# Kernel optimization log

Measured on AMD Instinct MI355X. Metric: run time of the kernel, lower is better.

## Reference

```python
import jax, jax.numpy as jnp
import numpy as np

D_MODEL = 256
D_INNER = 512   # expand=2 * d_model
D_STATE = 16
D_CONV = 4
DT_RANK = 16    # ceil(d_model/16)
N_BLOCKS = 5
BATCH = 8192
INPUT_DIM = 2048
NUM_CLASSES = 8


def setup_inputs() -> dict:
    key = jax.random.key(0)
    ks = jax.random.split(key, 10)
    rn = lambda k, shape, s: jax.random.normal(k, shape, jnp.float32) * s
    inp = {}
    inp['x'] = rn(ks[0], (BATCH, INPUT_DIM), 1.0)
    # preprocess Linear(input_dim, 256)
    inp['W_pre'] = rn(ks[1], (D_MODEL, INPUT_DIM), 0.02)
    inp['b_pre'] = jnp.zeros((D_MODEL,), jnp.float32)
    # per-block Mamba params, stacked over N_BLOCKS
    inp['in_proj_w'] = rn(ks[2], (N_BLOCKS, 2 * D_INNER, D_MODEL), 0.02)
    inp['conv_w'] = rn(ks[3], (N_BLOCKS, D_INNER, 1, D_CONV), 0.1)   # depthwise, groups=d_inner
    inp['conv_b'] = jnp.zeros((N_BLOCKS, D_INNER), jnp.float32)
    inp['x_proj_w'] = rn(ks[4], (N_BLOCKS, DT_RANK + 2 * D_STATE, D_INNER), 0.02)
    inp['dt_proj_w'] = rn(ks[5], (N_BLOCKS, D_INNER, DT_RANK), 0.1)
    inp['dt_proj_b'] = rn(ks[6], (N_BLOCKS, D_INNER), 0.1)
    # S4D-real init: A = 1..d_state, A_log = log(A)
    A = jnp.tile(jnp.arange(1, D_STATE + 1, dtype=jnp.float32)[None, None, :], (N_BLOCKS, D_INNER, 1))
    inp['A_log'] = jnp.log(A)
    inp['D'] = jnp.ones((N_BLOCKS, D_INNER), jnp.float32)
    inp['out_proj_w'] = rn(ks[7], (N_BLOCKS, D_MODEL, D_INNER), 0.02)
    inp['ln_g'] = jnp.ones((D_MODEL,), jnp.float32)
    inp['ln_b'] = jnp.zeros((D_MODEL,), jnp.float32)
    inp['W_cls'] = rn(ks[8], (NUM_CLASSES, D_MODEL), 0.02)
    inp['b_cls'] = jnp.zeros((NUM_CLASSES,), jnp.float32)
    return inp


def _mamba(x, in_w, cw, cb, xw, dtw, dtb, Alog, Dp, ow):
    # x: (B, L, d_model)
    B, L, _ = x.shape
    xz = jnp.einsum('bld,ed->ble', x, in_w)            # (B, L, 2*d_inner)
    xi, z = jnp.split(xz, 2, axis=-1)
    # causal depthwise conv1d over the sequence axis
    xt = xi.transpose(0, 2, 1)                         # (B, d_inner, L)
    xc = jax.lax.conv_general_dilated(
        xt, cw, window_strides=(1,), padding=[(D_CONV - 1, 0)],
        dimension_numbers=('NCH', 'OIH', 'NCH'), feature_group_count=D_INNER)
    xi = jax.nn.silu((xc + cb[None, :, None]).transpose(0, 2, 1))   # (B, L, d_inner)
    xdbl = jnp.einsum('bld,ed->ble', xi, xw)           # (B, L, dt_rank + 2*d_state)
    dt, Bm, Cm = jnp.split(xdbl, [DT_RANK, DT_RANK + D_STATE], axis=-1)
    dt = jax.nn.softplus(jnp.einsum('blr,dr->bld', dt, dtw) + dtb)  # (B, L, d_inner)
    A = -jnp.exp(Alog)                                  # (d_inner, d_state)
    dA = jnp.exp(dt[..., None] * A)                     # (B, L, d_inner, d_state)
    dBx = dt[..., None] * Bm[:, :, None, :] * xi[..., None]

    def step(h, t):
        dA_t, dBx_t, C_t = t
        h = dA_t * h + dBx_t                            # (B, d_inner, d_state)
        return h, jnp.einsum('bds,bs->bd', h, C_t)

    h0 = jnp.zeros((B, D_INNER, D_STATE), x.dtype)
    _, ys = jax.lax.scan(step, h0, (dA.swapaxes(0, 1), dBx.swapaxes(0, 1), Cm.swapaxes(0, 1)))
    y = ys.swapaxes(0, 1) + xi * Dp                     # (B, L, d_inner)
    y = y * jax.nn.silu(z)
    return jnp.einsum('bld,ed->ble', y, ow)             # (B, L, d_model)


def reference(x, W_pre, b_pre, in_proj_w, conv_w, conv_b, x_proj_w, dt_proj_w,
              dt_proj_b, A_log, D, out_proj_w, ln_g, ln_b, W_cls, b_cls):
    # dropout is identity in eval mode
    h = (x @ W_pre.T + b_pre)[:, None, :]               # (B, 1, 256)
    for i in range(N_BLOCKS):
        h = h + _mamba(h, in_proj_w[i], conv_w[i], conv_b[i], x_proj_w[i],
                       dt_proj_w[i], dt_proj_b[i], A_log[i], D[i], out_proj_w[i])
    mu = h.mean(-1, keepdims=True)
    var = ((h - mu) ** 2).mean(-1, keepdims=True)
    hn = (h - mu) * jax.lax.rsqrt(var + 1e-5) * ln_g + ln_b
    return hn[:, 0, :] @ W_cls.T + b_cls                # (B, num_classes)
```

## Files before the change

### kernel.cpp

```cpp
#include <hip/hip_runtime.h>
#include <hip/hip_bf16.h>

typedef __attribute__((ext_vector_type(8))) short bf16x8;
typedef __attribute__((ext_vector_type(4))) short s16x4;
typedef __attribute__((ext_vector_type(4))) float f32x4;
typedef __attribute__((ext_vector_type(4))) float float4v;

static __device__ __forceinline__ unsigned short f2b(float f) {
  unsigned int u = __builtin_bit_cast(unsigned int, f);
  u += 0x7fffu + ((u >> 16) & 1u);
  return (unsigned short)(u >> 16);
}
static __device__ __forceinline__ float b2f(unsigned short s) {
  unsigned int u = ((unsigned int)s) << 16;
  return __builtin_bit_cast(float, u);
}
static __device__ __forceinline__ float fsilu(float x) {
  float e = __builtin_amdgcn_exp2f(-1.44269504f * x);
  return x * __builtin_amdgcn_rcpf(1.f + e);
}
static __device__ __forceinline__ float fsoftplus(float a) {
  if (a > 20.f) return a;
  float t = __builtin_amdgcn_exp2f(1.44269504f * a);
  return 0.69314718f * __builtin_amdgcn_logf(1.f + t);
}
static __device__ __forceinline__ void gl16(const void* g, void* l) {
  __builtin_amdgcn_global_load_lds(
      (const __attribute__((address_space(1))) unsigned int*)g,
      (__attribute__((address_space(3))) unsigned int*)l, 16, 0, 0);
}
template <int N>
static __device__ __forceinline__ void waitv() {
  if constexpr (N == 0) asm volatile("s_waitcnt vmcnt(0)" ::: "memory");
  else if constexpr (N == 1) asm volatile("s_waitcnt vmcnt(1)" ::: "memory");
  else if constexpr (N == 2) asm volatile("s_waitcnt vmcnt(2)" ::: "memory");
  else if constexpr (N == 3) asm volatile("s_waitcnt vmcnt(3)" ::: "memory");
  else if constexpr (N == 4) asm volatile("s_waitcnt vmcnt(4)" ::: "memory");
  else if constexpr (N == 5) asm volatile("s_waitcnt vmcnt(5)" ::: "memory");
  else if constexpr (N == 6) asm volatile("s_waitcnt vmcnt(6)" ::: "memory");
  else if constexpr (N == 8) asm volatile("s_waitcnt vmcnt(8)" ::: "memory");
}
static __device__ __forceinline__ void lgkm_bar() {
  asm volatile("s_waitcnt lgkmcnt(0)" ::: "memory");
  __builtin_amdgcn_s_barrier();
}

template <int TM, int TN>
__global__ __launch_bounds__(256) void gemm_pl(
    const unsigned short* __restrict__ A, const unsigned short* __restrict__ W,
    int N, int K, int GY,
    const float* __restrict__ p0, float* __restrict__ of,
    unsigned short* __restrict__ ob) {
  constexpr int FM = TM / 32, FN = TN / 32;
  constexpr int IA = TM / 64, IW = TN / 64;
  constexpr int LPT = IA + IW;
  __shared__ __align__(16) unsigned short As[4][TM * 32];
  __shared__ __align__(16) unsigned short Ws[4][TN * 32];

  const int t = threadIdx.x, lane = t & 63, wave = t >> 6;
  const int lr = lane & 15;
  const int q = gridDim.x >> 3;
  const int s = (blockIdx.x & 7) * q + (blockIdx.x >> 3);
  const int bm = (s / GY) * TM, bn = (s % GY) * TN;
  const int wr = (wave >> 1) * (TM / 2), wc = (wave & 1) * (TN / 2);

  f32x4 acc[FM][FN];
#pragma unroll
  for (int i = 0; i < FM; ++i)
#pragma unroll
    for (int j = 0; j < FN; ++j) acc[i][j] = (f32x4){0.f, 0.f, 0.f, 0.f};

  const unsigned short* agB =
      A + (long)(bm + wave * (TM / 4) + (lane >> 2)) * K +
      ((lane & 3) ^ ((lane >> 3) & 3)) * 8;
  const unsigned short* wgB =
      W + (long)(bn + wave * (TN / 4) + (lane >> 2)) * K +
      ((lane & 3) ^ ((lane >> 3) & 3)) * 8;

  auto STAGE = [&](int k0, int b) {
#pragma unroll
    for (int j = 0; j < IA; ++j)
      gl16(agB + k0 + (long)j * 16 * K, &As[b][(wave * (TM / 4) + j * 16) * 32]);
#pragma unroll
    for (int j = 0; j < IW; ++j)
      gl16(wgB + k0 + (long)j * 16 * K, &Ws[b][(wave * (TN / 4) + j * 16) * 32]);
  };

  auto COMPUTE = [&](int b) {
    bf16x8 af[FM], bg[FN];
    const int sw = ((lane >> 4) ^ ((lane >> 1) & 3)) * 8;
#pragma unroll
    for (int m = 0; m < FM; ++m)
      af[m] = *(const bf16x8*)&As[b][(wr + m * 16 + lr) * 32 + sw];
#pragma unroll
    for (int n = 0; n < FN; ++n)
      bg[n] = *(const bf16x8*)&Ws[b][(wc + n * 16 + lr) * 32 + sw];
    __builtin_amdgcn_s_setprio(1);
#pragma unroll
    for (int m = 0; m < FM; ++m)
#pragma unroll
      for (int n = 0; n < FN; ++n)
        acc[m][n] = __builtin_amdgcn_mfma_f32_16x16x32_bf16(af[m], bg[n],
                                                            acc[m][n], 0, 0, 0);
    __builtin_amdgcn_s_setprio(0);
  };

  const int NT = K >> 5;
  STAGE(0, 0);
  STAGE(32, 1);
  for (int tt = 0; tt < NT; ++tt) {
    if (tt + 2 < NT) {
      STAGE((tt + 2) << 5, (tt + 2) & 3);
      waitv<2 * LPT>();
    } else if (tt + 1 < NT) {
      waitv<LPT>();
    } else {
      waitv<0>();
    }
    __builtin_amdgcn_s_barrier();
    COMPUTE(tt & 3);
    __builtin_amdgcn_sched_barrier(0);
  }

  const int m0 = bm + wr + (lane >> 4) * 4;
  const int n0 = bn + wc + lr;
#pragma unroll
  for (int mi = 0; mi < FM; ++mi)
#pragma unroll
    for (int ni = 0; ni < FN; ++ni) {
      const int n = n0 + ni * 16;
#pragma unroll
      for (int r = 0; r < 4; ++r) {
        const int m = m0 + mi * 16 + r;
        float v = acc[mi][ni][r] + p0[n];
        of[(long)m * N + n] = v;
        ob[(long)m * N + n] = f2b(v);
      }
    }
}

__global__ __launch_bounds__(512) void mamba5(
    const unsigned short* __restrict__ hb0, const float* __restrict__ h0,
    const unsigned short* __restrict__ inwb,
    const unsigned short* __restrict__ xwpb,
    const unsigned short* __restrict__ dtwpb,
    const unsigned short* __restrict__ owb,
    const float* __restrict__ conv_b, const float* __restrict__ dt_b,
    const float* __restrict__ Dp,
    const float* __restrict__ ln_g, const float* __restrict__ ln_b,
    const float* __restrict__ Wc, const float* __restrict__ bc,
    float* __restrict__ out) {
  __shared__ __align__(16) unsigned short SMEM[81216];
  unsigned short* XiL = SMEM;
  unsigned short* SzL = SMEM + 16384;
  unsigned short* Ring = SMEM + 32768;
  unsigned short* HLr = SMEM + 65536;
  float* Dxl = (float*)(SMEM + 73728);
  float* BCl = (float*)(SMEM + 78080);
  float* Par = (float*)(SMEM + 78144);

  const int t = threadIdx.x, lane = t & 63, w = t >> 6;
  const int lr = lane & 15, lg = lane >> 4;
  const int bm = blockIdx.x * 32;
  const int m04 = lg * 4;
  const int rg16 = (w >> 2) * 16;
  const int cg32 = (w & 3) * 32;
  const int strow = lane >> 2;
  const int stc = (lane & 3) ^ ((strow >> 1) & 3);

#pragma unroll
  for (int j = 0; j < 2; ++j) {
    const int i = w * 2 + j;
    const int row = 2 * i + (lane >> 5);
    const int c = (lane & 31) ^ (row & 7);
    gl16(hb0 + (long)(bm + row) * 256 + c * 8, HLr + i * 512);
  }
  float hres[2][2][4];
#pragma unroll
  for (int ng = 0; ng < 2; ++ng)
#pragma unroll
    for (int n = 0; n < 2; ++n)
#pragma unroll
      for (int r = 0; r < 4; ++r)
        hres[ng][n][r] = h0[(long)(bm + rg16 + m04 + r) * 256 + ng * 128 +
                            cg32 + n * 16 + lr];
  waitv<0>();
  __builtin_amdgcn_s_barrier();

  for (int blk = 0; blk < 5; ++blk) {
    const unsigned short* inw = inwb + (long)blk * 1024 * 256;
    const unsigned short* xwp = xwpb + (long)blk * 64 * 512;
    const unsigned short* dtwp = dtwpb + (long)blk * 512 * 32;
    const unsigned short* ow = owb + (long)blk * 256 * 512;
    const float* cbv = conv_b + blk * 512;
    const float* dtbv = dt_b + blk * 512;
    const float* Dv = Dp + blk * 512;

    auto STAGE1 = [&](int tt, int slot) {
      const int nt = tt >> 3, kq = tt & 7;
      gl16(inw + (long)(nt * 128 + w * 16 + strow) * 256 + kq * 32 + stc * 8,
           Ring + slot * 4096 + w * 512);
    };
    if (w < 6) {
      const float* ps = (w < 2) ? cbv + (w & 1) * 256
                      : (w < 4) ? dtbv + (w & 1) * 256
                                : Dv + (w & 1) * 256;
      gl16(ps + lane * 4, (unsigned short*)Par + w * 512);
    }
    STAGE1(0, 0); STAGE1(1, 1); STAGE1(2, 2); STAGE1(3, 3);
    STAGE1(4, 4); STAGE1(5, 5); STAGE1(6, 6);
    f32x4 acc1[2];
#pragma unroll
    for (int tt = 0; tt < 64; ++tt) {
      if (tt <= 57) waitv<6>();
      else if (tt == 58) waitv<5>();
      else if (tt == 59) waitv<4>();
      else if (tt == 60) waitv<3>();
      else if (tt == 61) waitv<2>();
      else if (tt == 62) waitv<1>();
      else waitv<0>();
      __builtin_amdgcn_s_barrier();
      if (tt + 7 < 64) STAGE1(tt + 7, (tt + 7) & 7);
      __builtin_amdgcn_sched_barrier(0);
      const int nt = tt >> 3, kq = tt & 7;
      if (kq == 0) {
#pragma unroll
        for (int n = 0; n < 2; ++n) {
          const int c = nt * 128 + cg32 + n * 16 + lr;
          const float cb = (nt < 4) ? Par[c] : 0.f;
          acc1[n] = (f32x4){cb, cb, cb, cb};
        }
      }
      const unsigned short* Bs = Ring + (tt & 7) * 4096;
      const int ar = rg16 + lr;
      bf16x8 af = *(const bf16x8*)
          &HLr[ar * 256 + (((kq * 4 + lg) ^ (ar & 7)) * 8)];
      bf16x8 bg[2];
#pragma unroll
      for (int n = 0; n < 2; ++n) {
        const int rb = cg32 + n * 16 + lr;
        bg[n] = *(const bf16x8*)&Bs[rb * 32 + ((lg ^ ((rb >> 1) & 3)) * 8)];
      }
      __builtin_amdgcn_s_setprio(1);
#pragma unroll
      for (int n = 0; n < 2; ++n)
        acc1[n] = __builtin_amdgcn_mfma_f32_16x16x32_bf16(af, bg[n], acc1[n],
                                                          0, 0, 0);
      __builtin_amdgcn_s_setprio(0);
      if (kq == 7) {
#pragma unroll
        for (int n = 0; n < 2; ++n) {
          const int c = nt * 128 + cg32 + n * 16 + lr;
#pragma unroll
          for (int r = 0; r < 4; ++r) {
            const int row = rg16 + m04 + r;
            const float v = fsilu(acc1[n][r]);
            if (nt < 4) {
              XiL[row * 512 + (((c >> 3) ^ (row & 7)) * 8) + (c & 7)] = f2b(v);
            } else {
              const int cs = c - 512;
              SzL[row * 512 + (((cs >> 3) ^ (row & 7)) * 8) + (cs & 7)] =
                  f2b(v);
            }
          }
        }
      }
      __builtin_amdgcn_sched_barrier(0);
    }
#pragma unroll
    for (int j = 0; j < 6; ++j) {
      const int i = w * 6 + j;
      gl16(xwp + (long)i * 512 + (lane ^ (i & 7)) * 8, Ring + i * 512);
    }
    lgkm_bar();

#pragma unroll
    for (int j = 0; j < 2; ++j) {
      const int u = w * 2 + j;
      const int row = u * 16 + (lane >> 2);
      const int c = (lane & 3) ^ (row & 3);
      gl16(dtwp + (long)row * 32 + c * 8, Ring + 24576 + u * 512);
    }
    waitv<2>();
    __builtin_amdgcn_s_barrier();
    {
      const int fm2 = w & 1, fn2 = w >> 1;
      const int ar = fm2 * 16 + lr, rb = fn2 * 16 + lr;
      f32x4 a2 = {0.f, 0.f, 0.f, 0.f};
      __builtin_amdgcn_s_setprio(1);
#pragma unroll
      for (int kc = 0; kc < 16; ++kc) {
        bf16x8 af = *(const bf16x8*)
            &XiL[ar * 512 + (((kc * 4 + lg) ^ (lr & 7)) * 8)];
        bf16x8 bg = *(const bf16x8*)
            &Ring[rb * 512 + (((kc * 4 + lg) ^ (lr & 7)) * 8)];
        a2 = __builtin_amdgcn_mfma_f32_16x16x32_bf16(af, bg, a2, 0, 0, 0);
      }
      __builtin_amdgcn_s_setprio(0);
#pragma unroll
      for (int r = 0; r < 4; ++r)
        Dxl[(fm2 * 16 + m04 + r) * 68 + fn2 * 16 + lr] = a2[r];
    }
    lgkm_bar();

#pragma unroll
    for (int j = 0; j < 2; ++j) {
      const int u = w * 2 + j;
      const int row = 256 + u * 16 + (lane >> 2);
      const int c = (lane & 3) ^ (row & 3);
      gl16(dtwp + (long)row * 32 + c * 8, Ring + u * 512);
    }
    if (t < 32) {
      float bc2 = 0.f;
      const float* dx = &Dxl[t * 68];
#pragma unroll
      for (int s2 = 0; s2 < 16; ++s2) bc2 += dx[16 + s2] * dx[32 + s2];
      BCl[t] = bc2;
    }
    bf16x8 afdt;
    {
      const float* dx = &Dxl[((w & 1) * 16 + lr) * 68 + lg * 8];
#pragma unroll
      for (int e = 0; e < 8; ++e) afdt[e] = (short)f2b(dx[e]);
    }
    waitv<0>();
    lgkm_bar();

    {
      const int fn4 = w >> 1, m04b = (w & 1) * 16 + m04;
#pragma unroll
      for (int tt = 0; tt < 8; ++tt) {
        const int d = tt * 64 + fn4 * 16 + lr;
        const unsigned short* dbase = (tt < 4) ? (Ring + 24576) : Ring;
        const int doff = (tt < 4) ? d : (d - 256);
        bf16x8 bg =
            *(const bf16x8*)&dbase[doff * 32 + ((lg ^ (d & 3)) * 8)];
        f32x4 da = __builtin_amdgcn_mfma_f32_16x16x32_bf16(
            afdt, bg, (f32x4){0.f, 0.f, 0.f, 0.f}, 0, 0, 0);
        const float dbv = Par[512 + d], dvv = Par[1024 + d];
#pragma unroll
        for (int r = 0; r < 4; ++r) {
          const int row = m04b + r;
          const float dtv = fsoftplus(da[r] + dbv);
          const int xoff = row * 512 + (((d >> 3) ^ (row & 7)) * 8) + (d & 7);
          const float y = b2f(XiL[xoff]) * (dtv * BCl[row] + dvv) *
                          b2f(SzL[xoff]);
          XiL[xoff] = f2b(y);
        }
      }
    }
    lgkm_bar();

    auto STAGE5 = [&](int tt, int slot) {
      const int ng = tt >> 4, kq = tt & 15;
      gl16(ow + (long)(ng * 128 + w * 16 + strow) * 512 + kq * 32 + stc * 8,
           Ring + slot * 4096 + w * 512);
    };
    STAGE5(0, 0); STAGE5(1, 1); STAGE5(2, 2); STAGE5(3, 3);
    STAGE5(4, 4); STAGE5(5, 5); STAGE5(6, 6);
    f32x4 acc5[2];
#pragma unroll
    for (int tt = 0; tt < 32; ++tt) {
      if (tt <= 25) waitv<6>();
      else if (tt == 26) waitv<5>();
      else if (tt == 27) waitv<4>();
      else if (tt == 28) waitv<3>();
      else if (tt == 29) waitv<2>();
      else if (tt == 30) waitv<1>();
      else waitv<0>();
      __builtin_amdgcn_s_barrier();
      if (tt + 7 < 32) STAGE5(tt + 7, (tt + 7) & 7);
      __builtin_amdgcn_sched_barrier(0);
      const int ng = tt >> 4, kq = tt & 15;
      if (kq == 0) {
        acc5[0] = (f32x4){0.f, 0.f, 0.f, 0.f};
        acc5[1] = (f32x4){0.f, 0.f, 0.f, 0.f};
      }
      const unsigned short* Bs = Ring + (tt & 7) * 4096;
      const int ar = rg16 + lr;
      bf16x8 af = *(const bf16x8*)
          &XiL[ar * 512 + (((kq * 4 + lg) ^ (ar & 7)) * 8)];
      bf16x8 bg[2];
#pragma unroll
      for (int n = 0; n < 2; ++n) {
        const int rb = cg32 + n * 16 + lr;
        bg[n] = *(const bf16x8*)&Bs[rb * 32 + ((lg ^ ((rb >> 1) & 3)) * 8)];
      }
      __builtin_amdgcn_s_setprio(1);
#pragma unroll
      for (int n = 0; n < 2; ++n)
        acc5[n] = __builtin_amdgcn_mfma_f32_16x16x32_bf16(af, bg[n], acc5[n],
                                                          0, 0, 0);
      __builtin_amdgcn_s_setprio(0);
      if (kq == 15) {
#pragma unroll
        for (int n = 0; n < 2; ++n) {
          const int col = ng * 128 + cg32 + n * 16 + lr;
#pragma unroll
          for (int r = 0; r < 4; ++r) {
            const int row = rg16 + m04 + r;
            const float v = acc5[n][r] + hres[ng][n][r];
            hres[ng][n][r] = v;
            HLr[row * 256 + (((col >> 3) ^ (row & 7)) * 8) + (col & 7)] =
                f2b(v);
          }
        }
      }
      __builtin_amdgcn_sched_barrier(0);
    }
    lgkm_bar();
  }

  {
    float* Rf = (float*)Ring;
#pragma unroll
    for (int ng = 0; ng < 2; ++ng)
#pragma unroll
      for (int n = 0; n < 2; ++n)
#pragma unroll
        for (int r = 0; r < 4; ++r)
          Rf[(rg16 + m04 + r) * 256 + ng * 128 + cg32 + n * 16 + lr] =
              hres[ng][n][r];
    lgkm_bar();
#pragma unroll
    for (int rr = 0; rr < 4; ++rr) {
      const int row = w * 4 + rr;
      float4v v = ((const float4v*)(Rf + row * 256))[lane];
      float s = v[0] + v[1] + v[2] + v[3];
#pragma unroll
      for (int o = 32; o; o >>= 1) s += __shfl_xor(s, o);
      const float mu = s * (1.f / 256.f);
      float d0 = v[0] - mu, d1 = v[1] - mu, d2 = v[2] - mu, d3 = v[3] - mu;
      float qq = d0 * d0 + d1 * d1 + d2 * d2 + d3 * d3;
#pragma unroll
      for (int o = 32; o; o >>= 1) qq += __shfl_xor(qq, o);
      const float rs = rsqrtf(qq * (1.f / 256.f) + 1e-5f);
      const float4v gv = ((const float4v*)ln_g)[lane];
      const float4v bv = ((const float4v*)ln_b)[lane];
      float hn[4];
      hn[0] = d0 * rs * gv[0] + bv[0];
      hn[1] = d1 * rs * gv[1] + bv[1];
      hn[2] = d2 * rs * gv[2] + bv[2];
      hn[3] = d3 * rs * gv[3] + bv[3];
      float lgt[8];
#pragma unroll
      for (int o = 0; o < 8; ++o) {
        const float4v wv = ((const float4v*)(Wc + o * 256))[lane];
        float p = hn[0] * wv[0] + hn[1] * wv[1] + hn[2] * wv[2] + hn[3] * wv[3];
#pragma unroll
        for (int x = 32; x; x >>= 1) p += __shfl_xor(p, x);
        lgt[o] = p;
      }
      if (lane == 0) {
#pragma unroll
        for (int o = 0; o < 8; ++o)
          out[(long)(bm + row) * 8 + o] = lgt[o] + bc[o];
      }
    }
  }
}

__global__ __launch_bounds__(256) void prep(
    const float* __restrict__ wpre, const float* __restrict__ inw,
    const float* __restrict__ ow, const float* __restrict__ xw,
    const float* __restrict__ dtw, const float* __restrict__ cw,
    const float* __restrict__ x,
    unsigned short* __restrict__ wpreb, unsigned short* __restrict__ inwb,
    unsigned short* __restrict__ owb, unsigned short* __restrict__ xwpb,
    unsigned short* __restrict__ dtwpb, unsigned short* __restrict__ xb) {
  if (blockIdx.x < 2672) {
    const int S0 = 524288;
    const int S1 = S0 + 1310720;
    const int S2 = S1 + 655360;
    const int S3 = S2 + 163840;
    const int S4 = S3 + 81920;
    int i4 = (blockIdx.x * 256 + threadIdx.x) * 4;
    if (i4 >= S4) return;
    float4v v = {0.f, 0.f, 0.f, 0.f};
    unsigned short* dst;
    if (i4 < S0) {
      v = *(const float4v*)(wpre + i4);
      dst = wpreb + i4;
    } else if (i4 < S1) {
      int o = i4 - S0;
      v = *(const float4v*)(inw + o);
      int b = o >> 18, row = (o >> 8) & 1023;
      if (row < 512) {
        float c3 = cw[(b * 512 + row) * 4 + 3];
        v[0] *= c3; v[1] *= c3; v[2] *= c3; v[3] *= c3;
      }
      dst = inwb + o;
    } else if (i4 < S2) {
      int o = i4 - S1;
      v = *(const float4v*)(ow + o);
      dst = owb + o;
    } else if (i4 < S3) {
      int o = i4 - S2;
      dst = xwpb + o;
      int k = o & 511, j = (o >> 9) & 63, b = o >> 15;
      if (j < 48) v = *(const float4v*)(xw + ((long)(b * 48 + j)) * 512 + k);
    } else {
      int o = i4 - S3;
      dst = dtwpb + o;
      int k = o & 31, dd = o >> 5;
      if (k < 16) v = *(const float4v*)(dtw + (long)dd * 16 + k);
    }
    s16x4 sv;
    sv[0] = (short)f2b(v[0]); sv[1] = (short)f2b(v[1]);
    sv[2] = (short)f2b(v[2]); sv[3] = (short)f2b(v[3]);
    *(s16x4*)dst = sv;
  } else {
    const int bid = blockIdx.x - 2672;
    const int n4 = (8192 * 2048) / 4;
    for (int i = bid * 256 + threadIdx.x; i < n4; i += 2048 * 256) {
      float4v v = ((const float4v*)x)[i];
      s16x4 o;
      o[0] = (short)f2b(v[0]); o[1] = (short)f2b(v[1]);
      o[2] = (short)f2b(v[2]); o[3] = (short)f2b(v[3]);
      ((s16x4*)xb)[i] = o;
    }
  }
}

extern "C" void kernel_launch(void* const* d_in, const int* in_sizes, int n_in,
                              void* d_out, int out_size, void* d_ws,
                              size_t ws_size, hipStream_t stream) {
  const float* x      = (const float*)d_in[0];
  const float* W_pre  = (const float*)d_in[1];
  const float* b_pre  = (const float*)d_in[2];
  const float* in_w   = (const float*)d_in[3];
  const float* conv_w = (const float*)d_in[4];
  const float* conv_b = (const float*)d_in[5];
  const float* x_w    = (const float*)d_in[6];
  const float* dt_w   = (const float*)d_in[7];
  const float* dt_b   = (const float*)d_in[8];
  const float* Dp     = (const float*)d_in[10];
  const float* out_w  = (const float*)d_in[11];
  const float* ln_g   = (const float*)d_in[12];
  const float* ln_b   = (const float*)d_in[13];
  const float* W_cls  = (const float*)d_in[14];
  const float* b_cls  = (const float*)d_in[15];
  float* out = (float*)d_out;

  char* w = (char*)d_ws;
  unsigned short* wpreb = (unsigned short*)w; w += 256 * 2048 * 2;
  unsigned short* inwb  = (unsigned short*)w; w += 5 * 1024 * 256 * 2;
  unsigned short* xwpb  = (unsigned short*)w; w += 5 * 64 * 512 * 2;
  unsigned short* owb   = (unsigned short*)w; w += 5 * 256 * 512 * 2;
  unsigned short* dtwpb = (unsigned short*)w; w += 5 * 512 * 32 * 2;
  float*          h     = (float*)w;          w += 8192 * 256 * 4;
  unsigned short* hb    = (unsigned short*)w; w += 8192 * 256 * 2;
  unsigned short* xb    = (unsigned short*)w; w += 8192 * 2048 * 2;

  prep<<<4720, 256, 0, stream>>>(W_pre, in_w, out_w, x_w, dt_w, conv_w, x,
                                 wpreb, inwb, owb, xwpb, dtwpb, xb);

  gemm_pl<128, 64><<<256, 256, 0, stream>>>(
      xb, wpreb, 256, 2048, 4, b_pre, h, hb);

  mamba5<<<256, 512, 0, stream>>>(hb, h, inwb, xwpb, dtwpb, owb,
                                  conv_b, dt_b, Dp,
                                  ln_g, ln_b, W_cls, b_cls, out);
}
```

Before: 181.1 us.

## Prefetch next block's in_proj weight tiles during out_proj stage

Moves the prologue loads of the first seven in_proj weight tiles for each Mamba block so they are issued at the end of the previous block's out_proj loop, with the very first block prefetched before the loop. This hides global load latency at block boundaries. Every wave now loads the per-block parameter vector, with waves 6 and 7 duplicating segments. The conv bias add moves from accumulator init to the epilogue so the Par read no longer stalls the first MMA step. The extra outstanding load changes the vmcnt accounting, hence waitv<7> for the early steps. Risks include ring buffer reuse hazards while the last out_proj iteration is still reading, and duplicate writes to Par.

```diff
diff --git a/kernel.cpp b/kernel.cpp
--- a/kernel.cpp
+++ b/kernel.cpp
@@ -38,6 +38,7 @@
   else if constexpr (N == 4) asm volatile("s_waitcnt vmcnt(4)" ::: "memory");
   else if constexpr (N == 5) asm volatile("s_waitcnt vmcnt(5)" ::: "memory");
   else if constexpr (N == 6) asm volatile("s_waitcnt vmcnt(6)" ::: "memory");
+  else if constexpr (N == 7) asm volatile("s_waitcnt vmcnt(7)" ::: "memory");
   else if constexpr (N == 8) asm volatile("s_waitcnt vmcnt(8)" ::: "memory");
 }
 static __device__ __forceinline__ void lgkm_bar() {
@@ -167,6 +168,7 @@
   const int cg32 = (w & 3) * 32;
   const int strow = lane >> 2;
   const int stc = (lane & 3) ^ ((strow >> 1) & 3);
+  const int seg = (w < 6) ? w : (w - 2);
 
 #pragma unroll
   for (int j = 0; j < 2; ++j) {
@@ -186,6 +188,11 @@
                             cg32 + n * 16 + lr];
   waitv<0>();
   __builtin_amdgcn_s_barrier();
+
+#pragma unroll
+  for (int j = 0; j < 7; ++j)
+    gl16(inwb + (long)(w * 16 + strow) * 256 + j * 32 + stc * 8,
+         Ring + j * 4096 + w * 512);
 
   for (int blk = 0; blk < 5; ++blk) {
     const unsigned short* inw = inwb + (long)blk * 1024 * 256;
@@ -196,23 +203,23 @@
     const float* dtbv = dt_b + blk * 512;
     const float* Dv = Dp + blk * 512;
 
+    {
+      const float* ps = (seg < 2) ? cbv + (seg & 1) * 256
+                      : (seg < 4) ? dtbv + (seg & 1) * 256
+                                  : Dv + (seg & 1) * 256;
+      gl16(ps + lane * 4, (unsigned short*)Par + seg * 512);
+    }
+
     auto STAGE1 = [&](int tt, int slot) {
       const int nt = tt >> 3, kq = tt & 7;
       gl16(inw + (long)(nt * 128 + w * 16 + strow) * 256 + kq * 32 + stc * 8,
            Ring + slot * 4096 + w * 512);
     };
-    if (w < 6) {
-      const float* ps = (w < 2) ? cbv + (w & 1) * 256
-                      : (w < 4) ? dtbv + (w & 1) * 256
-                                : Dv + (w & 1) * 256;
-      gl16(ps + lane * 4, (unsigned short*)Par + w * 512);
-    }
-    STAGE1(0, 0); STAGE1(1, 1); STAGE1(2, 2); STAGE1(3, 3);
-    STAGE1(4, 4); STAGE1(5, 5); STAGE1(6, 6);
     f32x4 acc1[2];
 #pragma unroll
     for (int tt = 0; tt < 64; ++tt) {
-      if (tt <= 57) waitv<6>();
+      if (tt < 7) waitv<7>();
+      else if (tt <= 57) waitv<6>();
       else if (tt == 58) waitv<5>();
       else if (tt == 59) waitv<4>();
       else if (tt == 60) waitv<3>();
@@ -224,12 +231,8 @@
       __builtin_amdgcn_sched_barrier(0);
       const int nt = tt >> 3, kq = tt & 7;
       if (kq == 0) {
-#pragma unroll
-        for (int n = 0; n < 2; ++n) {
-          const int c = nt * 128 + cg32 + n * 16 + lr;
-          const float cb = (nt < 4) ? Par[c] : 0.f;
-          acc1[n] = (f32x4){cb, cb, cb, cb};
-        }
+        acc1[0] = (f32x4){0.f, 0.f, 0.f, 0.f};
+        acc1[1] = (f32x4){0.f, 0.f, 0.f, 0.f};
       }
       const unsigned short* Bs = Ring + (tt & 7) * 4096;
       const int ar = rg16 + lr;
@@ -251,10 +254,11 @@
 #pragma unroll
         for (int n = 0; n < 2; ++n) {
           const int c = nt * 128 + cg32 + n * 16 + lr;
+          const float cb = (nt < 4) ? Par[c] : 0.f;
 #pragma unroll
           for (int r = 0; r < 4; ++r) {
             const int row = rg16 + m04 + r;
-            const float v = fsilu(acc1[n][r]);
+            const float v = fsilu(acc1[n][r] + cb);
             if (nt < 4) {
               XiL[row * 512 + (((c >> 3) ^ (row & 7)) * 8) + (c & 7)] = f2b(v);
             } else {
@@ -407,6 +411,13 @@
         }
       }
       __builtin_amdgcn_sched_barrier(0);
+    }
+    if (blk < 4) {
+      const unsigned short* inw_n = inwb + (long)(blk + 1) * 1024 * 256;
+#pragma unroll
+      for (int j = 0; j < 7; ++j)
+        gl16(inw_n + (long)(w * 16 + strow) * 256 + j * 32 + stc * 8,
+             Ring + j * 4096 + w * 512);
     }
     lgkm_bar();
   }
```

New measurement: 207.0 us. +14.3%, slower.
